# Kernel tuning notes

Hardware: AMD Instinct MI355X
Metric: run time of the kernel (lower is better)

## Reference

```python
import jax, jax.numpy as jnp
import numpy as np

NUM_GRAPHS = 1024

def setup_inputs() -> dict:
    key = jax.random.key(0)
    ks = jax.random.split(key, 6)
    N, E = 500000, 16000000
    x = jax.random.normal(ks[0], (N, 4), dtype=jnp.float32)
    edge_index = jax.random.randint(ks[1], (2, E), 0, N, dtype=jnp.int32)
    batch = jnp.sort(jax.random.randint(ks[2], (N,), 0, NUM_GRAPHS, dtype=jnp.int32))
    eps = jnp.zeros((), dtype=jnp.float32)
    W1 = jax.random.normal(ks[3], (4, 16), dtype=jnp.float32) * 0.5
    b1 = jnp.zeros((16,), dtype=jnp.float32)
    W2 = jax.random.normal(ks[4], (16, 4), dtype=jnp.float32) * 0.25
    b2 = jnp.zeros((4,), dtype=jnp.float32)
    return {"x": x, "edge_index": edge_index, "batch": batch,
            "eps": eps, "W1": W1, "b1": b1, "W2": W2, "b2": b2}

def reference(x, edge_index, batch, eps, W1, b1, W2, b2):
    N = x.shape[0]
    src, dst = edge_index[0], edge_index[1]
    # GINConv aggregation: sum of neighbor (source) features at each target node
    agg = jax.ops.segment_sum(x[src], dst, num_segments=N)  # [N, 4]
    h = (1.0 + eps) * x + agg
    # 2-layer MLP: Lin(4,16) -> ReLU -> Lin(16,4)
    h = jax.nn.relu(h @ W1 + b1) @ W2 + b2
    h = jax.nn.relu(h)
    # global_mean_pool over batch segment ids
    sums = jax.ops.segment_sum(h, batch, num_segments=NUM_GRAPHS)      # [G, 4]
    cnts = jax.ops.segment_sum(jnp.ones((N,), h.dtype), batch, num_segments=NUM_GRAPHS)
    pooled = sums / jnp.maximum(cnts, 1.0)[:, None]
    return jax.nn.log_softmax(pooled, axis=1)
```

## Files before the change

### kernel.cpp

```cpp
#include <hip/hip_runtime.h>

#define NUM_GRAPHS 1024
#define BIN_BITS 10
#define BIN_SIZE (1 << BIN_BITS)
#define EB 8192
#define STH 512
#define EPT 16
#define ATH 1024
#define ACH 8192
#define AEPT (ACH / ATH)

__global__ void init_kernel(int* __restrict__ cursor, float* __restrict__ gsum,
                            float* __restrict__ gcnt, int cap) {
    int t = threadIdx.x;
    if (t < 512) cursor[t] = t * cap;
    for (int j = t; j < NUM_GRAPHS * 4; j += 1024) gsum[j] = 0.0f;
    for (int j = t; j < NUM_GRAPHS; j += 1024) gcnt[j] = 0.0f;
}

__device__ inline unsigned bf16_rn(float f) {
    unsigned u = __float_as_uint(f);
    return (u + 0x7FFFu + ((u >> 16) & 1u)) >> 16;
}
__global__ void x_to_bf16_kernel(const float4* __restrict__ x,
                                 uint2* __restrict__ x16, int N) {
    int i = blockIdx.x * blockDim.x + threadIdx.x;
    if (i >= N) return;
    float4 v = x[i];
    uint2 r;
    r.x = bf16_rn(v.x) | (bf16_rn(v.y) << 16);
    r.y = bf16_rn(v.z) | (bf16_rn(v.w) << 16);
    x16[i] = r;
}

__global__ void __launch_bounds__(STH) bin_scatter(const int* __restrict__ src,
                                                   const int* __restrict__ dst,
                                                   int* __restrict__ packed,
                                                   int* __restrict__ cursor,
                                                   int E, int cap, int nb) {
    __shared__ int shist[512];
    __shared__ int sprefix[513];
    __shared__ int sgbase[512];
    __shared__ int spacked[EB];
    __shared__ int wsum[8];

    const int t = threadIdx.x;
    const int lane = t & 63;
    const int wave = t >> 6;
    const int b0 = blockIdx.x * EB;
    const int myBase = b0 + t * EPT;

    for (int j = t; j < 512; j += STH) shist[j] = 0;
    __syncthreads();

    int pv[EPT];
    int bl[EPT];
    const bool full = (myBase + EPT <= E);
    if (full) {
#pragma unroll
        for (int v = 0; v < EPT / 4; ++v) {
            int4 d = *(const int4*)(dst + myBase + v * 4);
            int4 s = *(const int4*)(src + myBase + v * 4);
            int bn, lp;
            bn = ((unsigned)d.x) >> BIN_BITS; lp = atomicAdd(&shist[bn], 1);
            pv[v * 4 + 0] = ((d.x & (BIN_SIZE - 1)) << 19) | s.x;
            bl[v * 4 + 0] = (bn << 13) | lp;
            bn = ((unsigned)d.y) >> BIN_BITS; lp = atomicAdd(&shist[bn], 1);
            pv[v * 4 + 1] = ((d.y & (BIN_SIZE - 1)) << 19) | s.y;
            bl[v * 4 + 1] = (bn << 13) | lp;
            bn = ((unsigned)d.z) >> BIN_BITS; lp = atomicAdd(&shist[bn], 1);
            pv[v * 4 + 2] = ((d.z & (BIN_SIZE - 1)) << 19) | s.z;
            bl[v * 4 + 2] = (bn << 13) | lp;
            bn = ((unsigned)d.w) >> BIN_BITS; lp = atomicAdd(&shist[bn], 1);
            pv[v * 4 + 3] = ((d.w & (BIN_SIZE - 1)) << 19) | s.w;
            bl[v * 4 + 3] = (bn << 13) | lp;
        }
    } else {
#pragma unroll
        for (int i = 0; i < EPT; ++i) {
            int e = myBase + i;
            bool ok = e < E;
            int d = ok ? dst[e] : 0;
            int s = ok ? src[e] : 0;
            int bn = ((unsigned)d) >> BIN_BITS;
            int lp = 0;
            if (ok) lp = atomicAdd(&shist[bn], 1);
            pv[i] = ((d & (BIN_SIZE - 1)) << 19) | s;
            bl[i] = ok ? ((bn << 13) | lp) : -1;
        }
    }
    __syncthreads();

    {
        int v = shist[t];
        int inc = v;
#pragma unroll
        for (int off = 1; off < 64; off <<= 1) {
            int u = __shfl_up(inc, off);
            if (lane >= off) inc += u;
        }
        if (lane == 63) wsum[wave] = inc;
        __syncthreads();
        if (t == 0) {
            int acc = 0;
#pragma unroll
            for (int w = 0; w < 8; ++w) { int c = wsum[w]; wsum[w] = acc; acc += c; }
        }
        __syncthreads();
        sprefix[t + 1] = inc + wsum[wave];
        if (t == 0) sprefix[0] = 0;
        if (t < nb && v > 0) sgbase[t] = atomicAdd(&cursor[t], v);
    }
    __syncthreads();

    if (full) {
#pragma unroll
        for (int i = 0; i < EPT; ++i) {
            int bn = ((unsigned)bl[i]) >> 13;
            int lp = bl[i] & 0x1FFF;
            spacked[sprefix[bn] + lp] = pv[i];
        }
    } else {
#pragma unroll
        for (int i = 0; i < EPT; ++i) {
            if (bl[i] >= 0) {
                int bn = ((unsigned)bl[i]) >> 13;
                int lp = bl[i] & 0x1FFF;
                spacked[sprefix[bn] + lp] = pv[i];
            }
        }
    }
    __syncthreads();

    int cnt = sprefix[nb < 512 ? nb : 512];
    int totE = E - b0; if (totE < 0) totE = 0;
    if (cnt > totE) cnt = totE;
    for (int j = t; j < cnt; j += STH) {
        int lo = 0, hi = nb;
        while (hi - lo > 1) {
            int mid = (lo + hi) >> 1;
            if (sprefix[mid] <= j) lo = mid; else hi = mid;
        }
        int pos = sgbase[lo] + (j - sprefix[lo]);
        if (pos < (lo + 1) * cap)
            __builtin_nontemporal_store(spacked[j], &packed[pos]);
    }
}

__global__ void __launch_bounds__(ATH) bin_accum_mlp_pool(
        const float4* __restrict__ x,
        const uint2* __restrict__ x16,
        const int* __restrict__ packed,
        const int* __restrict__ cursor,
        const int* __restrict__ batch,
        const float* __restrict__ eps_p,
        const float* __restrict__ W1, const float* __restrict__ b1,
        const float* __restrict__ W2, const float* __restrict__ b2,
        float* __restrict__ gsum, float* __restrict__ gcnt,
        int N, int cap) {
    __shared__ int srt[ACH];
    __shared__ int hist[BIN_SIZE];
    __shared__ int pfx[BIN_SIZE + 1];
    __shared__ int wsum[16];

    const int bin = blockIdx.x;
    const int t = threadIdx.x;
    const int lane = t & 63;
    const int wave = t >> 6;

    const int start = bin * cap;
    int end = cursor[bin];
    if (end > start + cap) end = start + cap;

    float a0 = 0.f, a1 = 0.f, a2 = 0.f, a3 = 0.f;

#pragma unroll 1
    for (int cs = start; cs < end; cs += ACH) {
        int ce = cs + ACH; if (ce > end) ce = end;

        hist[t] = 0;
        __syncthreads();

        int dlp[AEPT];
        int sv[AEPT];
#pragma unroll
        for (int i = 0; i < AEPT; ++i) {
            int e = cs + i * ATH + t;
            bool ok = e < ce;
            int p = ok ? __builtin_nontemporal_load(&packed[e]) : 0;
            int dl = ((unsigned)p) >> 19;
            int lp = 0;
            if (ok) lp = atomicAdd(&hist[dl], 1);
            dlp[i] = ok ? ((dl << 13) | lp) : -1;
            sv[i] = p & 0x7FFFF;
        }
        __syncthreads();

        {
            int v = hist[t];
            int inc = v;
#pragma unroll
            for (int off = 1; off < 64; off <<= 1) {
                int u = __shfl_up(inc, off);
                if (lane >= off) inc += u;
            }
            if (lane == 63) wsum[wave] = inc;
            __syncthreads();
            if (t == 0) {
                int acc = 0;
#pragma unroll
                for (int w = 0; w < 16; ++w) { int c = wsum[w]; wsum[w] = acc; acc += c; }
            }
            __syncthreads();
            pfx[t + 1] = inc + wsum[wave];
            if (t == 0) pfx[0] = 0;
        }
        __syncthreads();

#pragma unroll
        for (int i = 0; i < AEPT; ++i) {
            if (dlp[i] >= 0) {
                int dl = ((unsigned)dlp[i]) >> 13;
                int lp = dlp[i] & 0x1FFF;
                srt[pfx[dl] + lp] = sv[i];
            }
        }
        __syncthreads();

        int jb = pfx[t], je = pfx[t + 1];
        for (int j = jb; j < je; ++j) {
            uint2 v = x16[srt[j]];
            a0 += __uint_as_float(v.x << 16);
            a1 += __uint_as_float(v.x & 0xFFFF0000u);
            a2 += __uint_as_float(v.y << 16);
            a3 += __uint_as_float(v.y & 0xFFFF0000u);
        }
        __syncthreads();
    }

    int n = bin * BIN_SIZE + t;
    bool valid = n < N;
    float o0 = 0.f, o1 = 0.f, o2 = 0.f, o3 = 0.f;
    int g = -1;
    if (valid) {
        float eps = eps_p[0];
        float4 xv = x[n];
        float h0 = (1.0f + eps) * xv.x + a0;
        float h1 = (1.0f + eps) * xv.y + a1;
        float h2 = (1.0f + eps) * xv.z + a2;
        float h3 = (1.0f + eps) * xv.w + a3;

        float tmp[16];
#pragma unroll
        for (int j = 0; j < 16; ++j) {
            float v = b1[j] + h0 * W1[j] + h1 * W1[16 + j] + h2 * W1[32 + j] + h3 * W1[48 + j];
            tmp[j] = v > 0.0f ? v : 0.0f;
        }
        float o[4];
#pragma unroll
        for (int j = 0; j < 4; ++j) {
            float v = b2[j];
#pragma unroll
            for (int k = 0; k < 16; ++k) v += tmp[k] * W2[k * 4 + j];
            o[j] = v > 0.0f ? v : 0.0f;
        }
        o0 = o[0]; o1 = o[1]; o2 = o[2]; o3 = o[3];
        g = batch[n];
    }

    int g0 = __shfl(g, 0);
    bool uni = __all(g == g0);
    if (uni && g0 >= 0) {
#pragma unroll
        for (int off = 32; off > 0; off >>= 1) {
            o0 += __shfl_down(o0, off);
            o1 += __shfl_down(o1, off);
            o2 += __shfl_down(o2, off);
            o3 += __shfl_down(o3, off);
        }
        if ((t & 63) == 0) {
            unsafeAtomicAdd(&gsum[(size_t)g0 * 4 + 0], o0);
            unsafeAtomicAdd(&gsum[(size_t)g0 * 4 + 1], o1);
            unsafeAtomicAdd(&gsum[(size_t)g0 * 4 + 2], o2);
            unsafeAtomicAdd(&gsum[(size_t)g0 * 4 + 3], o3);
            unsafeAtomicAdd(&gcnt[g0], 64.0f);
        }
    } else if (valid) {
        unsafeAtomicAdd(&gsum[(size_t)g * 4 + 0], o0);
        unsafeAtomicAdd(&gsum[(size_t)g * 4 + 1], o1);
        unsafeAtomicAdd(&gsum[(size_t)g * 4 + 2], o2);
        unsafeAtomicAdd(&gsum[(size_t)g * 4 + 3], o3);
        unsafeAtomicAdd(&gcnt[g], 1.0f);
    }
}

__global__ void pool_softmax_kernel(const float* __restrict__ gsum,
                                    const float* __restrict__ gcnt,
                                    float* __restrict__ out) {
    int g = blockIdx.x * blockDim.x + threadIdx.x;
    if (g >= NUM_GRAPHS) return;
    float c = fmaxf(gcnt[g], 1.0f);
    float p0 = gsum[g * 4 + 0] / c;
    float p1 = gsum[g * 4 + 1] / c;
    float p2 = gsum[g * 4 + 2] / c;
    float p3 = gsum[g * 4 + 3] / c;
    float m = fmaxf(fmaxf(p0, p1), fmaxf(p2, p3));
    float s = expf(p0 - m) + expf(p1 - m) + expf(p2 - m) + expf(p3 - m);
    float lse = m + logf(s);
    out[g * 4 + 0] = p0 - lse;
    out[g * 4 + 1] = p1 - lse;
    out[g * 4 + 2] = p2 - lse;
    out[g * 4 + 3] = p3 - lse;
}

__global__ void edge_scatter_kernel(const float4* __restrict__ x,
                                    const int* __restrict__ src,
                                    const int* __restrict__ dst,
                                    float* __restrict__ agg,
                                    int E) {
    int t = blockIdx.x * blockDim.x + threadIdx.x;
    int e = t * 4;
    if (e + 3 < E) {
        int4 s = *(const int4*)(src + e);
        int4 d = *(const int4*)(dst + e);
        float4 xv;
        xv = x[s.x];
        unsafeAtomicAdd(&agg[(size_t)d.x * 4 + 0], xv.x);
        unsafeAtomicAdd(&agg[(size_t)d.x * 4 + 1], xv.y);
        unsafeAtomicAdd(&agg[(size_t)d.x * 4 + 2], xv.z);
        unsafeAtomicAdd(&agg[(size_t)d.x * 4 + 3], xv.w);
        xv = x[s.y];
        unsafeAtomicAdd(&agg[(size_t)d.y * 4 + 0], xv.x);
        unsafeAtomicAdd(&agg[(size_t)d.y * 4 + 1], xv.y);
        unsafeAtomicAdd(&agg[(size_t)d.y * 4 + 2], xv.z);
        unsafeAtomicAdd(&agg[(size_t)d.y * 4 + 3], xv.w);
        xv = x[s.z];
        unsafeAtomicAdd(&agg[(size_t)d.z * 4 + 0], xv.x);
        unsafeAtomicAdd(&agg[(size_t)d.z * 4 + 1], xv.y);
        unsafeAtomicAdd(&agg[(size_t)d.z * 4 + 2], xv.z);
        unsafeAtomicAdd(&agg[(size_t)d.z * 4 + 3], xv.w);
        xv = x[s.w];
        unsafeAtomicAdd(&agg[(size_t)d.w * 4 + 0], xv.x);
        unsafeAtomicAdd(&agg[(size_t)d.w * 4 + 1], xv.y);
        unsafeAtomicAdd(&agg[(size_t)d.w * 4 + 2], xv.z);
        unsafeAtomicAdd(&agg[(size_t)d.w * 4 + 3], xv.w);
    } else {
        for (int i = e; i < E; ++i) {
            int sv = src[i], dv = dst[i];
            float4 xv = x[sv];
            unsafeAtomicAdd(&agg[(size_t)dv * 4 + 0], xv.x);
            unsafeAtomicAdd(&agg[(size_t)dv * 4 + 1], xv.y);
            unsafeAtomicAdd(&agg[(size_t)dv * 4 + 2], xv.z);
            unsafeAtomicAdd(&agg[(size_t)dv * 4 + 3], xv.w);
        }
    }
}

__global__ void node_mlp_pool_kernel(const float4* __restrict__ x,
                                     const float4* __restrict__ agg,
                                     const int* __restrict__ batch,
                                     const float* __restrict__ eps_p,
                                     const float* __restrict__ W1,
                                     const float* __restrict__ b1,
                                     const float* __restrict__ W2,
                                     const float* __restrict__ b2,
                                     float* __restrict__ gsum,
                                     float* __restrict__ gcnt,
                                     int N) {
    int i = blockIdx.x * blockDim.x + threadIdx.x;
    bool valid = i < N;
    float o0 = 0.f, o1 = 0.f, o2 = 0.f, o3 = 0.f;
    int g = -1;
    if (valid) {
        float eps = eps_p[0];
        float4 xv = x[i];
        float4 av = agg[i];
        float h0 = (1.0f + eps) * xv.x + av.x;
        float h1 = (1.0f + eps) * xv.y + av.y;
        float h2 = (1.0f + eps) * xv.z + av.z;
        float h3 = (1.0f + eps) * xv.w + av.w;
        float tmp[16];
#pragma unroll
        for (int j = 0; j < 16; ++j) {
            float v = b1[j] + h0 * W1[j] + h1 * W1[16 + j] + h2 * W1[32 + j] + h3 * W1[48 + j];
            tmp[j] = v > 0.0f ? v : 0.0f;
        }
        float o[4];
#pragma unroll
        for (int j = 0; j < 4; ++j) {
            float v = b2[j];
#pragma unroll
            for (int k = 0; k < 16; ++k) v += tmp[k] * W2[k * 4 + j];
            o[j] = v > 0.0f ? v : 0.0f;
        }
        o0 = o[0]; o1 = o[1]; o2 = o[2]; o3 = o[3];
        g = batch[i];
    }
    int g0 = __shfl(g, 0);
    bool uni = __all(g == g0);
    if (uni && g0 >= 0) {
#pragma unroll
        for (int off = 32; off > 0; off >>= 1) {
            o0 += __shfl_down(o0, off);
            o1 += __shfl_down(o1, off);
            o2 += __shfl_down(o2, off);
            o3 += __shfl_down(o3, off);
        }
        if ((threadIdx.x & 63) == 0) {
            unsafeAtomicAdd(&gsum[(size_t)g0 * 4 + 0], o0);
            unsafeAtomicAdd(&gsum[(size_t)g0 * 4 + 1], o1);
            unsafeAtomicAdd(&gsum[(size_t)g0 * 4 + 2], o2);
            unsafeAtomicAdd(&gsum[(size_t)g0 * 4 + 3], o3);
            unsafeAtomicAdd(&gcnt[g0], 64.0f);
        }
    } else if (valid) {
        unsafeAtomicAdd(&gsum[(size_t)g * 4 + 0], o0);
        unsafeAtomicAdd(&gsum[(size_t)g * 4 + 1], o1);
        unsafeAtomicAdd(&gsum[(size_t)g * 4 + 2], o2);
        unsafeAtomicAdd(&gsum[(size_t)g * 4 + 3], o3);
        unsafeAtomicAdd(&gcnt[g], 1.0f);
    }
}

extern "C" void kernel_launch(void* const* d_in, const int* in_sizes, int n_in,
                              void* d_out, int out_size, void* d_ws, size_t ws_size,
                              hipStream_t stream) {
    const float* x     = (const float*)d_in[0];
    const int*   ei    = (const int*)d_in[1];
    const int*   batch = (const int*)d_in[2];
    const float* eps   = (const float*)d_in[3];
    const float* W1    = (const float*)d_in[4];
    const float* b1    = (const float*)d_in[5];
    const float* W2    = (const float*)d_in[6];
    const float* b2    = (const float*)d_in[7];

    const int N = in_sizes[0] / 4;
    const int E = in_sizes[1] / 2;
    const int* src = ei;
    const int* dst = ei + (size_t)E;

    const int nb = (N + BIN_SIZE - 1) >> BIN_BITS;
    const int epb = (E + nb - 1) / nb;
    const int cap = epb + epb / 8 + 1024;

    size_t x16_elems = ((size_t)2 * N + 3) & ~(size_t)3;
    size_t packed_elems = ((size_t)nb * cap + 3) & ~(size_t)3;
    size_t need = (x16_elems + packed_elems + 512 + NUM_GRAPHS * 5) * sizeof(float);

    if (nb <= 512 && N < (1 << 19) && need <= ws_size) {
        uint2* x16    = (uint2*)d_ws;
        int*   packed = (int*)d_ws + x16_elems;
        int*   cursor = packed + packed_elems;
        float* gsum   = (float*)(cursor + 512);
        float* gcnt   = gsum + (size_t)NUM_GRAPHS * 4;

        init_kernel<<<1, 1024, 0, stream>>>(cursor, gsum, gcnt, cap);

        x_to_bf16_kernel<<<(N + 511) / 512, 512, 0, stream>>>(
            (const float4*)x, x16, N);

        int nblocks_e = (E + EB - 1) / EB;
        bin_scatter<<<nblocks_e, STH, 0, stream>>>(src, dst, packed, cursor, E, cap, nb);

        bin_accum_mlp_pool<<<nb, ATH, 0, stream>>>(
            (const float4*)x, (const uint2*)x16, packed, cursor, batch, eps,
            W1, b1, W2, b2, gsum, gcnt, N, cap);

        pool_softmax_kernel<<<(NUM_GRAPHS + 255) / 256, 256, 0, stream>>>(
            gsum, gcnt, (float*)d_out);
    } else {
        float* agg  = (float*)d_ws;
        float* gsum = agg + (size_t)N * 4;
        float* gcnt = gsum + (size_t)NUM_GRAPHS * 4;
        size_t zero_bytes = ((size_t)N * 4 + NUM_GRAPHS * 5) * sizeof(float);
        (void)hipMemsetAsync(d_ws, 0, zero_bytes, stream);

        int e4 = (E + 3) / 4;
        edge_scatter_kernel<<<(e4 + 255) / 256, 256, 0, stream>>>(
            (const float4*)x, src, dst, agg, E);

        node_mlp_pool_kernel<<<(N + 255) / 256, 256, 0, stream>>>(
            (const float4*)x, (const float4*)agg, batch, eps, W1, b1, W2, b2,
            gsum, gcnt, N);

        pool_softmax_kernel<<<(NUM_GRAPHS + 255) / 256, 256, 0, stream>>>(
            gsum, gcnt, (float*)d_out);
    }
}
```

Before: 480.7 us.

## Fuse init into bf16 prep, record bin ids in LDS, vectorize packed loads

Merges the init and bf16-conversion kernels into one launch. In bin_scatter, each sorted slot's bin id is stored in a shared ushort array, so the per-element binary search over the prefix array goes away. In the accumulate kernel, packed edges are read as 16-byte nontemporal vector loads; cap is rounded up to a multiple of 4 so those loads stay aligned. The extra 16KB of LDS in bin_scatter may reduce its occupancy.

```diff
diff --git a/kernel.cpp b/kernel.cpp
--- a/kernel.cpp
+++ b/kernel.cpp
@@ -10,27 +10,27 @@
 #define ACH 8192
 #define AEPT (ACH / ATH)
 
-__global__ void init_kernel(int* __restrict__ cursor, float* __restrict__ gsum,
-                            float* __restrict__ gcnt, int cap) {
-    int t = threadIdx.x;
-    if (t < 512) cursor[t] = t * cap;
-    for (int j = t; j < NUM_GRAPHS * 4; j += 1024) gsum[j] = 0.0f;
-    for (int j = t; j < NUM_GRAPHS; j += 1024) gcnt[j] = 0.0f;
-}
+typedef int v4i __attribute__((ext_vector_type(4)));
 
 __device__ inline unsigned bf16_rn(float f) {
     unsigned u = __float_as_uint(f);
     return (u + 0x7FFFu + ((u >> 16) & 1u)) >> 16;
 }
-__global__ void x_to_bf16_kernel(const float4* __restrict__ x,
-                                 uint2* __restrict__ x16, int N) {
+__global__ void prep_kernel(const float4* __restrict__ x, uint2* __restrict__ x16,
+                            int N, int* __restrict__ cursor,
+                            float* __restrict__ gsum, float* __restrict__ gcnt,
+                            int cap) {
     int i = blockIdx.x * blockDim.x + threadIdx.x;
-    if (i >= N) return;
-    float4 v = x[i];
-    uint2 r;
-    r.x = bf16_rn(v.x) | (bf16_rn(v.y) << 16);
-    r.y = bf16_rn(v.z) | (bf16_rn(v.w) << 16);
-    x16[i] = r;
+    if (i < 512) cursor[i] = i * cap;
+    if (i < NUM_GRAPHS * 4) gsum[i] = 0.0f;
+    if (i < NUM_GRAPHS) gcnt[i] = 0.0f;
+    if (i < N) {
+        float4 v = x[i];
+        uint2 r;
+        r.x = bf16_rn(v.x) | (bf16_rn(v.y) << 16);
+        r.y = bf16_rn(v.z) | (bf16_rn(v.w) << 16);
+        x16[i] = r;
+    }
 }
 
 __global__ void __launch_bounds__(STH) bin_scatter(const int* __restrict__ src,
@@ -42,6 +42,7 @@
     __shared__ int sprefix[513];
     __shared__ int sgbase[512];
     __shared__ int spacked[EB];
+    __shared__ unsigned short sbin[EB];
     __shared__ int wsum[8];
 
     const int t = threadIdx.x;
@@ -118,7 +119,9 @@
         for (int i = 0; i < EPT; ++i) {
             int bn = ((unsigned)bl[i]) >> 13;
             int lp = bl[i] & 0x1FFF;
-            spacked[sprefix[bn] + lp] = pv[i];
+            int idx = sprefix[bn] + lp;
+            spacked[idx] = pv[i];
+            sbin[idx] = (unsigned short)bn;
         }
     } else {
 #pragma unroll
@@ -126,7 +129,9 @@
             if (bl[i] >= 0) {
                 int bn = ((unsigned)bl[i]) >> 13;
                 int lp = bl[i] & 0x1FFF;
-                spacked[sprefix[bn] + lp] = pv[i];
+                int idx = sprefix[bn] + lp;
+                spacked[idx] = pv[i];
+                sbin[idx] = (unsigned short)bn;
             }
         }
     }
@@ -136,13 +141,9 @@
     int totE = E - b0; if (totE < 0) totE = 0;
     if (cnt > totE) cnt = totE;
     for (int j = t; j < cnt; j += STH) {
-        int lo = 0, hi = nb;
-        while (hi - lo > 1) {
-            int mid = (lo + hi) >> 1;
-            if (sprefix[mid] <= j) lo = mid; else hi = mid;
-        }
-        int pos = sgbase[lo] + (j - sprefix[lo]);
-        if (pos < (lo + 1) * cap)
+        int bn = sbin[j];
+        int pos = sgbase[bn] + (j - sprefix[bn]);
+        if (pos < (bn + 1) * cap)
             __builtin_nontemporal_store(spacked[j], &packed[pos]);
     }
 }
@@ -184,15 +185,27 @@
         int dlp[AEPT];
         int sv[AEPT];
 #pragma unroll
-        for (int i = 0; i < AEPT; ++i) {
-            int e = cs + i * ATH + t;
-            bool ok = e < ce;
-            int p = ok ? __builtin_nontemporal_load(&packed[e]) : 0;
-            int dl = ((unsigned)p) >> 19;
-            int lp = 0;
-            if (ok) lp = atomicAdd(&hist[dl], 1);
-            dlp[i] = ok ? ((dl << 13) | lp) : -1;
-            sv[i] = p & 0x7FFFF;
+        for (int i = 0; i < AEPT / 4; ++i) {
+            int ebase = cs + (i * ATH + t) * 4;
+            v4i p4;
+            if (ebase + 3 < ce) {
+                p4 = __builtin_nontemporal_load((const v4i*)(packed + ebase));
+            } else {
+                p4.x = (ebase + 0 < ce) ? packed[ebase + 0] : 0;
+                p4.y = (ebase + 1 < ce) ? packed[ebase + 1] : 0;
+                p4.z = (ebase + 2 < ce) ? packed[ebase + 2] : 0;
+                p4.w = (ebase + 3 < ce) ? packed[ebase + 3] : 0;
+            }
+#pragma unroll
+            for (int k = 0; k < 4; ++k) {
+                int p = (k == 0) ? p4.x : (k == 1) ? p4.y : (k == 2) ? p4.z : p4.w;
+                bool ok = (ebase + k) < ce;
+                int dl = ((unsigned)p) >> 19;
+                int lp = 0;
+                if (ok) lp = atomicAdd(&hist[dl], 1);
+                dlp[i * 4 + k] = ok ? ((dl << 13) | lp) : -1;
+                sv[i * 4 + k] = p & 0x7FFFF;
+            }
         }
         __syncthreads();
 
@@ -441,7 +454,8 @@
 
     const int nb = (N + BIN_SIZE - 1) >> BIN_BITS;
     const int epb = (E + nb - 1) / nb;
-    const int cap = epb + epb / 8 + 1024;
+    int cap = epb + epb / 8 + 1024;
+    cap = (cap + 3) & ~3;
 
     size_t x16_elems = ((size_t)2 * N + 3) & ~(size_t)3;
     size_t packed_elems = ((size_t)nb * cap + 3) & ~(size_t)3;
@@ -454,10 +468,8 @@
         float* gsum   = (float*)(cursor + 512);
         float* gcnt   = gsum + (size_t)NUM_GRAPHS * 4;
 
-        init_kernel<<<1, 1024, 0, stream>>>(cursor, gsum, gcnt, cap);
-
-        x_to_bf16_kernel<<<(N + 511) / 512, 512, 0, stream>>>(
-            (const float4*)x, x16, N);
+        prep_kernel<<<(N + 511) / 512, 512, 0, stream>>>(
+            (const float4*)x, x16, N, cursor, gsum, gcnt, cap);
 
         int nblocks_e = (E + EB - 1) / EB;
         bin_scatter<<<nblocks_e, STH, 0, stream>>>(src, dst, packed, cursor, E, cap, nb);
```

Measured after the change: 450.1 us. -6.4%, faster.
